# Optimization experiments

Hardware: AMD Instinct MI355X
Metric: run time of the kernel (lower is better)

## Reference

```python
import jax, jax.numpy as jnp
import numpy as np

DIM = 1024
NUM_HEADS = 16
HEAD_DIM = DIM // NUM_HEADS


def setup_inputs() -> dict:
    key = jax.random.key(0)
    k1, k2, k3 = jax.random.split(key, 3)
    x = jax.random.normal(k1, (4, 1024, DIM), dtype=jnp.float32)
    # match nn.Linear init scale roughly: small weights
    Wqkv = jax.random.normal(k2, (3 * DIM, DIM), dtype=jnp.float32) * (1.0 / np.sqrt(DIM))
    Wproj = jax.random.normal(k3, (DIM, DIM), dtype=jnp.float32) * (1.0 / np.sqrt(DIM))
    bproj = jnp.zeros((DIM,), dtype=jnp.float32)
    return {"x": x, "Wqkv": Wqkv, "Wproj": Wproj, "bproj": bproj}


def reference(x, Wqkv, Wproj, bproj):
    bsz, tsz, chans = x.shape
    # fused QKV projection (qkv_bias=False): [B,T,3C]
    qkv = jnp.einsum("btc,oc->bto", x, Wqkv)
    qkv = qkv.reshape(bsz, tsz, 3, NUM_HEADS, HEAD_DIM)
    q = qkv[:, :, 0].transpose(0, 2, 1, 3)  # [B,H,T,D]
    k = qkv[:, :, 1].transpose(0, 2, 1, 3)
    v = qkv[:, :, 2].transpose(0, 2, 1, 3)
    scale = 1.0 / np.sqrt(HEAD_DIM)
    logits = jnp.einsum("bhqd,bhkd->bhqk", q, k) * scale  # [B,H,T,T]
    attn = jax.nn.softmax(logits, axis=-1)
    out = jnp.einsum("bhqk,bhkd->bhqd", attn, v)  # [B,H,T,D]
    out = out.transpose(0, 2, 1, 3).reshape(bsz, tsz, chans)
    return jnp.einsum("btc,oc->bto", out, Wproj) + bproj
```

## Files before the change

### kernel.cpp

```cpp
#include <hip/hip_runtime.h>
#include <hip/hip_bf16.h>

typedef __attribute__((ext_vector_type(8))) short bfrag8;
typedef __attribute__((ext_vector_type(4))) short bfrag4;
typedef __attribute__((ext_vector_type(4))) float floatx4;

typedef unsigned short ushort_t;
typedef unsigned int uint_t;

static __device__ __forceinline__ uint_t pk_bf16(float a, float b) {
    union { __hip_bfloat162 h; uint_t u; } cv;
    cv.h = __float22bfloat162_rn(make_float2(a, b));
    return cv.u;
}

#if __has_builtin(__builtin_amdgcn_mfma_f32_16x16x16_bf16)
static __device__ __forceinline__ floatx4 mfma16(bfrag4 a, bfrag4 b, floatx4 c) {
    return __builtin_amdgcn_mfma_f32_16x16x16_bf16(a, b, c, 0, 0, 0);
}
#elif __has_builtin(__builtin_amdgcn_mfma_f32_16x16x16bf16_1k)
static __device__ __forceinline__ floatx4 mfma16(bfrag4 a, bfrag4 b, floatx4 c) {
    return __builtin_amdgcn_mfma_f32_16x16x16bf16_1k(a, b, c, 0, 0, 0);
}
#else
static __device__ __forceinline__ floatx4 mfma16(bfrag4 a, bfrag4 b, floatx4 c) {
    bfrag8 az = {a[0], 0, a[1], 0, a[2], 0, a[3], 0};
    bfrag8 bz = {b[0], 0, b[1], 0, b[2], 0, b[3], 0};
    return __builtin_amdgcn_mfma_f32_16x16x32_bf16(az, bz, c, 0, 0, 0);
}
#endif

static __device__ __forceinline__ void gl_lds16(const ushort_t* g, ushort_t* l) {
    __builtin_amdgcn_global_load_lds(
        (const __attribute__((address_space(1))) void*)g,
        (__attribute__((address_space(3))) void*)l, 16, 0, 0);
}

__global__ __launch_bounds__(256)
void cvt_all(const float* __restrict__ x, const float* __restrict__ wqkv,
             const float* __restrict__ wproj, ushort_t* __restrict__ xb,
             ushort_t* __restrict__ wqkvb, ushort_t* __restrict__ wprojb) {
    int blk = blockIdx.x;
    const float* src; ushort_t* dst; int base;
    if (blk < 4096)      { src = x;     dst = xb;     base = blk; }
    else if (blk < 7168) { src = wqkv;  dst = wqkvb;  base = blk - 4096; }
    else                 { src = wproj; dst = wprojb; base = blk - 7168; }
    int i = (base * 256 + threadIdx.x) * 4;
    float4 f = *(const float4*)(src + i);
    uint_t lo = pk_bf16(f.x, f.y);
    uint_t hi = pk_bf16(f.z, f.w);
    uint2 u = {lo, hi};
    *(uint2*)(dst + i) = u;
}

__global__ __launch_bounds__(256, 2)
void qkv_gemm(const ushort_t* __restrict__ A, const ushort_t* __restrict__ B,
              ushort_t* __restrict__ qp, ushort_t* __restrict__ kp,
              ushort_t* __restrict__ vp) {
    const int K = 1024;
    __shared__ ushort_t As[128 * 64];
    __shared__ ushort_t Bs[128 * 64];
    int tid = threadIdx.x;
    int wave = __builtin_amdgcn_readfirstlane(tid >> 6);
    int lane = tid & 63;
    int quad = lane >> 4, l16 = lane & 15;
    int wm = (wave >> 1) * 64, wn = (wave & 1) * 64;
    int m0 = blockIdx.y * 128, n0 = blockIdx.x * 128;

    int rl = lane >> 3;
    int gc = (lane & 7) ^ rl;

    floatx4 acc[4][4] = {};

    const ushort_t* Ag = A + (size_t)m0 * K;
    const ushort_t* Bg = B + (size_t)n0 * K;

    for (int k0 = 0; k0 < K; k0 += 64) {
        __syncthreads();
#pragma unroll
        for (int i = 0; i < 4; i++) {
            int row = wave * 32 + i * 8 + rl;
            gl_lds16(Ag + (size_t)row * K + k0 + gc * 8, &As[(wave * 32 + i * 8) * 64]);
            gl_lds16(Bg + (size_t)row * K + k0 + gc * 8, &Bs[(wave * 32 + i * 8) * 64]);
        }
        __syncthreads();
#pragma unroll
        for (int ks = 0; ks < 2; ks++) {
            bfrag8 af[4], bf[4];
#pragma unroll
            for (int mt = 0; mt < 4; mt++) {
                int r = wm + mt * 16 + l16;
                af[mt] = *(const bfrag8*)&As[r * 64 + ((4 * ks + quad) ^ (r & 7)) * 8];
            }
#pragma unroll
            for (int nt = 0; nt < 4; nt++) {
                int r = wn + nt * 16 + l16;
                bf[nt] = *(const bfrag8*)&Bs[r * 64 + ((4 * ks + quad) ^ (r & 7)) * 8];
            }
#pragma unroll
            for (int mt = 0; mt < 4; mt++)
#pragma unroll
                for (int nt = 0; nt < 4; nt++)
                    acc[mt][nt] = __builtin_amdgcn_mfma_f32_16x16x32_bf16(
                        af[mt], bf[nt], acc[mt][nt], 0, 0, 0);
        }
    }

#pragma unroll
    for (int mt = 0; mt < 4; mt++) {
#pragma unroll
        for (int nt = 0; nt < 4; nt++) {
            int o = n0 + wn + nt * 16 + l16;
            int s = o >> 10;
            int rem = o & 1023;
            int h = rem >> 6, d = rem & 63;
            ushort_t* dst = (s == 0) ? qp : (s == 1) ? kp : vp;
            float scl = (s == 0) ? 0.125f : 1.0f;
            uint_t p01 = pk_bf16(acc[mt][nt][0] * scl, acc[mt][nt][1] * scl);
            uint_t p23 = pk_bf16(acc[mt][nt][2] * scl, acc[mt][nt][3] * scl);
            ushort_t pv[4] = {(ushort_t)p01, (ushort_t)(p01 >> 16),
                              (ushort_t)p23, (ushort_t)(p23 >> 16)};
#pragma unroll
            for (int r = 0; r < 4; r++) {
                int t = m0 + wm + mt * 16 + quad * 4 + r;
                int b = t >> 10, tt = t & 1023;
                dst[((size_t)(b * 16 + h) * 1024 + tt) * 64 + d] = pv[r];
            }
        }
    }
}

__global__ __launch_bounds__(256)
void transpose_v(const ushort_t* __restrict__ v, ushort_t* __restrict__ vT) {
    int bh = blockIdx.y;
    int t0 = blockIdx.x * 64;
    __shared__ ushort_t tile[64][72];
    int tid = threadIdx.x;
    int r = tid >> 3;
    int c = (tid & 7) * 8;
#pragma unroll
    for (int i = 0; i < 2; i++) {
        int t = r + i * 32;
        *(uint4*)&tile[t][c] = *(const uint4*)&v[((size_t)bh * 1024 + t0 + t) * 64 + c];
    }
    __syncthreads();
#pragma unroll
    for (int i = 0; i < 2; i++) {
        int d = r + i * 32;
        union { ushort_t u[8]; uint4 v4; } tmp;
#pragma unroll
        for (int j = 0; j < 8; j++) tmp.u[j] = tile[c + j][d];
        *(uint4*)&vT[((size_t)bh * 64 + d) * 1024 + t0 + c] = tmp.v4;
    }
}

__global__ __launch_bounds__(256, 2)
void attn_kernel(const ushort_t* __restrict__ q, const ushort_t* __restrict__ k,
                 const ushort_t* __restrict__ vT, ushort_t* __restrict__ out) {
    int id = blockIdx.x;
    int bh = (id & 7) + ((id >> 6) << 3);
    int qt = (id >> 3) & 7;
    const ushort_t* qb = q + (size_t)bh * 1024 * 64;
    const ushort_t* kb = k + (size_t)bh * 1024 * 64;
    const ushort_t* vtb = vT + (size_t)bh * 64 * 1024;
    int tid = threadIdx.x;
    int wave = __builtin_amdgcn_readfirstlane(tid >> 6);
    int lane = tid & 63;
    int quad = lane >> 4, l16 = lane & 15;
    int q0 = qt * 128 + wave * 32;

    __shared__ ushort_t Ks[128 * 64];
    __shared__ ushort_t VTs[64 * 136];

    int rl = lane >> 3;
    int gc = (lane & 7) ^ rl;

    bfrag8 qf[2][2];
#pragma unroll
    for (int mt = 0; mt < 2; mt++)
#pragma unroll
        for (int ks = 0; ks < 2; ks++)
            qf[mt][ks] = *(const bfrag8*)&qb[(size_t)(q0 + mt * 16 + l16) * 64 + ks * 32 + quad * 8];

    floatx4 oacc[2][4] = {};
    float li[2] = {0.f, 0.f};

    int vd = tid >> 2;
    int vc = tid & 3;

    for (int kt = 0; kt < 8; kt++) {
        uint4 vv[4];
#pragma unroll
        for (int i = 0; i < 4; i++)
            vv[i] = *(const uint4*)&vtb[(size_t)vd * 1024 + kt * 128 + (vc + i * 4) * 8];
        __syncthreads();
#pragma unroll
        for (int i = 0; i < 4; i++) {
            int row = wave * 32 + i * 8 + rl;
            gl_lds16(kb + (size_t)(kt * 128 + row) * 64 + gc * 8, &Ks[(wave * 32 + i * 8) * 64]);
        }
#pragma unroll
        for (int i = 0; i < 4; i++)
            *(uint4*)&VTs[vd * 136 + (vc + i * 4) * 8] = vv[i];
        __syncthreads();

#pragma unroll
        for (int half = 0; half < 2; half++) {
            floatx4 st[2][4] = {};
#pragma unroll
            for (int ks = 0; ks < 2; ks++) {
                bfrag8 kf[4];
#pragma unroll
                for (int tt = 0; tt < 4; tt++) {
                    int r = (half * 4 + tt) * 16 + l16;
                    kf[tt] = *(const bfrag8*)&Ks[r * 64 + ((4 * ks + quad) ^ (r & 7)) * 8];
                }
#pragma unroll
                for (int mt = 0; mt < 2; mt++)
#pragma unroll
                    for (int tt = 0; tt < 4; tt++)
                        st[mt][tt] = __builtin_amdgcn_mfma_f32_16x16x32_bf16(
                            kf[tt], qf[mt][ks], st[mt][tt], 0, 0, 0);
            }

            bfrag4 pf[2][4];
#pragma unroll
            for (int mt = 0; mt < 2; mt++)
#pragma unroll
                for (int tt = 0; tt < 4; tt++) {
                    float p0 = __expf(st[mt][tt][0]);
                    float p1 = __expf(st[mt][tt][1]);
                    float p2 = __expf(st[mt][tt][2]);
                    float p3 = __expf(st[mt][tt][3]);
                    li[mt] += (p0 + p1) + (p2 + p3);
                    union { uint2 u; bfrag4 f; } pk;
                    pk.u.x = pk_bf16(p0, p1);
                    pk.u.y = pk_bf16(p2, p3);
                    pf[mt][tt] = pk.f;
                }

#pragma unroll
            for (int tt = 0; tt < 4; tt++) {
                int keyoff = (half * 4 + tt) * 16;
                bfrag4 vb[4];
#pragma unroll
                for (int nd = 0; nd < 4; nd++)
                    vb[nd] = *(const bfrag4*)&VTs[(nd * 16 + l16) * 136 + keyoff + quad * 4];
#pragma unroll
                for (int mt = 0; mt < 2; mt++)
#pragma unroll
                    for (int nd = 0; nd < 4; nd++)
                        oacc[mt][nd] = mfma16(pf[mt][tt], vb[nd], oacc[mt][nd]);
            }
        }
    }

    float inv[2][4];
#pragma unroll
    for (int mt = 0; mt < 2; mt++) {
        float s0 = li[mt];
        s0 += __shfl_xor(s0, 16);
        s0 += __shfl_xor(s0, 32);
#pragma unroll
        for (int r = 0; r < 4; r++)
            inv[mt][r] = 1.0f / __shfl(s0, quad * 4 + r);
    }

    int b = bh >> 4, h = bh & 15;
#pragma unroll
    for (int mt = 0; mt < 2; mt++)
#pragma unroll
        for (int nd = 0; nd < 4; nd++) {
            uint_t c01 = pk_bf16(oacc[mt][nd][0] * inv[mt][0], oacc[mt][nd][1] * inv[mt][1]);
            uint_t c23 = pk_bf16(oacc[mt][nd][2] * inv[mt][2], oacc[mt][nd][3] * inv[mt][3]);
            ushort_t pv[4] = {(ushort_t)c01, (ushort_t)(c01 >> 16),
                              (ushort_t)c23, (ushort_t)(c23 >> 16)};
#pragma unroll
            for (int r = 0; r < 4; r++) {
                int t = q0 + mt * 16 + quad * 4 + r;
                int c = h * 64 + nd * 16 + l16;
                out[((size_t)(b * 1024 + t)) * 1024 + c] = pv[r];
            }
        }
}

__global__ __launch_bounds__(256, 2)
void proj_gemm(const ushort_t* __restrict__ A, const ushort_t* __restrict__ B,
               const float* __restrict__ bias, float* __restrict__ out) {
    const int K = 1024;
    __shared__ ushort_t As[64 * 64];
    __shared__ ushort_t Bs[128 * 64];
    int tid = threadIdx.x;
    int wave = __builtin_amdgcn_readfirstlane(tid >> 6);
    int lane = tid & 63;
    int quad = lane >> 4, l16 = lane & 15;
    int wm = (wave >> 1) * 32, wn = (wave & 1) * 64;
    int m0 = blockIdx.y * 64, n0 = blockIdx.x * 128;

    int rl = lane >> 3;
    int gc = (lane & 7) ^ rl;

    floatx4 acc[2][4] = {};

    const ushort_t* Ag = A + (size_t)m0 * K;
    const ushort_t* Bg = B + (size_t)n0 * K;

    for (int k0 = 0; k0 < K; k0 += 64) {
        __syncthreads();
#pragma unroll
        for (int i = 0; i < 2; i++) {
            int row = wave * 16 + i * 8 + rl;
            gl_lds16(Ag + (size_t)row * K + k0 + gc * 8, &As[(wave * 16 + i * 8) * 64]);
        }
#pragma unroll
        for (int i = 0; i < 4; i++) {
            int row = wave * 32 + i * 8 + rl;
            gl_lds16(Bg + (size_t)row * K + k0 + gc * 8, &Bs[(wave * 32 + i * 8) * 64]);
        }
        __syncthreads();
#pragma unroll
        for (int ks = 0; ks < 2; ks++) {
            bfrag8 af[2], bf[4];
#pragma unroll
            for (int mt = 0; mt < 2; mt++) {
                int r = wm + mt * 16 + l16;
                af[mt] = *(const bfrag8*)&As[r * 64 + ((4 * ks + quad) ^ (r & 7)) * 8];
            }
#pragma unroll
            for (int nt = 0; nt < 4; nt++) {
                int r = wn + nt * 16 + l16;
                bf[nt] = *(const bfrag8*)&Bs[r * 64 + ((4 * ks + quad) ^ (r & 7)) * 8];
            }
#pragma unroll
            for (int mt = 0; mt < 2; mt++)
#pragma unroll
                for (int nt = 0; nt < 4; nt++)
                    acc[mt][nt] = __builtin_amdgcn_mfma_f32_16x16x32_bf16(
                        af[mt], bf[nt], acc[mt][nt], 0, 0, 0);
        }
    }

#pragma unroll
    for (int mt = 0; mt < 2; mt++) {
#pragma unroll
        for (int nt = 0; nt < 4; nt++) {
            int o = n0 + wn + nt * 16 + l16;
            float bv = bias[o];
#pragma unroll
            for (int r = 0; r < 4; r++) {
                int t = m0 + wm + mt * 16 + quad * 4 + r;
                out[(size_t)t * 1024 + o] = acc[mt][nt][r] + bv;
            }
        }
    }
}

extern "C" void kernel_launch(void* const* d_in, const int* in_sizes, int n_in,
                              void* d_out, int out_size, void* d_ws, size_t ws_size,
                              hipStream_t stream) {
    const float* x     = (const float*)d_in[0];
    const float* Wqkv  = (const float*)d_in[1];
    const float* Wproj = (const float*)d_in[2];
    const float* bproj = (const float*)d_in[3];
    float* out = (float*)d_out;

    char* ws = (char*)d_ws;
    ushort_t* xb     = (ushort_t*)(ws);
    ushort_t* wqkvb  = (ushort_t*)(ws + ((size_t)8 << 20));
    ushort_t* wprojb = (ushort_t*)(ws + ((size_t)14 << 20));
    ushort_t* qp     = (ushort_t*)(ws + ((size_t)16 << 20));
    ushort_t* kp     = (ushort_t*)(ws + ((size_t)24 << 20));
    ushort_t* vp     = (ushort_t*)(ws + ((size_t)32 << 20));
    ushort_t* vTp    = (ushort_t*)(ws + ((size_t)40 << 20));
    ushort_t* attn   = (ushort_t*)(ws + ((size_t)48 << 20));

    cvt_all<<<8192, 256, 0, stream>>>(x, Wqkv, Wproj, xb, wqkvb, wprojb);
    qkv_gemm<<<dim3(24, 32), 256, 0, stream>>>(xb, wqkvb, qp, kp, vp);
    transpose_v<<<dim3(16, 64), 256, 0, stream>>>(vp, vTp);
    attn_kernel<<<512, 256, 0, stream>>>(qp, kp, vTp, attn);
    proj_gemm<<<dim3(8, 64), 256, 0, stream>>>(attn, wprojb, bproj, out);
}
```

Before: 169.1 us.

## Fuse V transpose into QKV GEMM epilogue and drop transpose kernel

The QKV GEMM epilogue now writes V directly in transposed [B,H,D,T] layout with 8-byte packed stores, so the separate transpose_v kernel and its round trip through global memory go away. Q/K blocks take a uniform per-block branch instead of per-element selection. The launch bounds hint rises to 3 blocks per CU, and the VT shared-memory row padding shrinks from 136 to 132. The risks are register spills from the tighter occupancy target and changed LDS bank-conflict behaviour in the attention kernel.

```diff
diff --git a/kernel.cpp b/kernel.cpp
--- a/kernel.cpp
+++ b/kernel.cpp
@@ -7,6 +7,7 @@
 
 typedef unsigned short ushort_t;
 typedef unsigned int uint_t;
+typedef unsigned long long u64_t;
 
 static __device__ __forceinline__ uint_t pk_bf16(float a, float b) {
     union { __hip_bfloat162 h; uint_t u; } cv;
@@ -53,10 +54,10 @@
     *(uint2*)(dst + i) = u;
 }
 
-__global__ __launch_bounds__(256, 2)
+__global__ __launch_bounds__(256, 3)
 void qkv_gemm(const ushort_t* __restrict__ A, const ushort_t* __restrict__ B,
               ushort_t* __restrict__ qp, ushort_t* __restrict__ kp,
-              ushort_t* __restrict__ vp) {
+              ushort_t* __restrict__ vTp) {
     const int K = 1024;
     __shared__ ushort_t As[128 * 64];
     __shared__ ushort_t Bs[128 * 64];
@@ -106,51 +107,43 @@
         }
     }
 
-#pragma unroll
-    for (int mt = 0; mt < 4; mt++) {
-#pragma unroll
-        for (int nt = 0; nt < 4; nt++) {
-            int o = n0 + wn + nt * 16 + l16;
-            int s = o >> 10;
-            int rem = o & 1023;
-            int h = rem >> 6, d = rem & 63;
-            ushort_t* dst = (s == 0) ? qp : (s == 1) ? kp : vp;
-            float scl = (s == 0) ? 0.125f : 1.0f;
-            uint_t p01 = pk_bf16(acc[mt][nt][0] * scl, acc[mt][nt][1] * scl);
-            uint_t p23 = pk_bf16(acc[mt][nt][2] * scl, acc[mt][nt][3] * scl);
-            ushort_t pv[4] = {(ushort_t)p01, (ushort_t)(p01 >> 16),
-                              (ushort_t)p23, (ushort_t)(p23 >> 16)};
-#pragma unroll
-            for (int r = 0; r < 4; r++) {
-                int t = m0 + wm + mt * 16 + quad * 4 + r;
-                int b = t >> 10, tt = t & 1023;
-                dst[((size_t)(b * 16 + h) * 1024 + tt) * 64 + d] = pv[r];
-            }
-        }
-    }
-}
-
-__global__ __launch_bounds__(256)
-void transpose_v(const ushort_t* __restrict__ v, ushort_t* __restrict__ vT) {
-    int bh = blockIdx.y;
-    int t0 = blockIdx.x * 64;
-    __shared__ ushort_t tile[64][72];
-    int tid = threadIdx.x;
-    int r = tid >> 3;
-    int c = (tid & 7) * 8;
-#pragma unroll
-    for (int i = 0; i < 2; i++) {
-        int t = r + i * 32;
-        *(uint4*)&tile[t][c] = *(const uint4*)&v[((size_t)bh * 1024 + t0 + t) * 64 + c];
-    }
-    __syncthreads();
-#pragma unroll
-    for (int i = 0; i < 2; i++) {
-        int d = r + i * 32;
-        union { ushort_t u[8]; uint4 v4; } tmp;
-#pragma unroll
-        for (int j = 0; j < 8; j++) tmp.u[j] = tile[c + j][d];
-        *(uint4*)&vT[((size_t)bh * 64 + d) * 1024 + t0 + c] = tmp.v4;
+    int s = n0 >> 10;
+    if (s < 2) {
+        ushort_t* dst = (s == 0) ? qp : kp;
+        float scl = (s == 0) ? 0.125f : 1.0f;
+#pragma unroll
+        for (int mt = 0; mt < 4; mt++) {
+#pragma unroll
+            for (int nt = 0; nt < 4; nt++) {
+                int o = (n0 & 1023) + wn + nt * 16 + l16;
+                int h = o >> 6, d = o & 63;
+                uint_t p01 = pk_bf16(acc[mt][nt][0] * scl, acc[mt][nt][1] * scl);
+                uint_t p23 = pk_bf16(acc[mt][nt][2] * scl, acc[mt][nt][3] * scl);
+                ushort_t pv[4] = {(ushort_t)p01, (ushort_t)(p01 >> 16),
+                                  (ushort_t)p23, (ushort_t)(p23 >> 16)};
+#pragma unroll
+                for (int r = 0; r < 4; r++) {
+                    int t = m0 + wm + mt * 16 + quad * 4 + r;
+                    int b = t >> 10, tt = t & 1023;
+                    dst[((size_t)(b * 16 + h) * 1024 + tt) * 64 + d] = pv[r];
+                }
+            }
+        }
+    } else {
+#pragma unroll
+        for (int mt = 0; mt < 4; mt++) {
+            int t = m0 + wm + mt * 16 + quad * 4;
+            int b = t >> 10, tt = t & 1023;
+#pragma unroll
+            for (int nt = 0; nt < 4; nt++) {
+                int o = (n0 & 1023) + wn + nt * 16 + l16;
+                int h = o >> 6, d = o & 63;
+                uint_t p01 = pk_bf16(acc[mt][nt][0], acc[mt][nt][1]);
+                uint_t p23 = pk_bf16(acc[mt][nt][2], acc[mt][nt][3]);
+                u64_t pk = ((u64_t)p23 << 32) | p01;
+                *(u64_t*)&vTp[((size_t)(b * 16 + h) * 64 + d) * 1024 + tt] = pk;
+            }
+        }
     }
 }
 
@@ -170,7 +163,7 @@
     int q0 = qt * 128 + wave * 32;
 
     __shared__ ushort_t Ks[128 * 64];
-    __shared__ ushort_t VTs[64 * 136];
+    __shared__ ushort_t VTs[64 * 132];
 
     int rl = lane >> 3;
     int gc = (lane & 7) ^ rl;
@@ -201,7 +194,7 @@
         }
 #pragma unroll
         for (int i = 0; i < 4; i++)
-            *(uint4*)&VTs[vd * 136 + (vc + i * 4) * 8] = vv[i];
+            *(uint4*)&VTs[vd * 132 + (vc + i * 4) * 8] = vv[i];
         __syncthreads();
 
 #pragma unroll
@@ -245,7 +238,7 @@
                 bfrag4 vb[4];
 #pragma unroll
                 for (int nd = 0; nd < 4; nd++)
-                    vb[nd] = *(const bfrag4*)&VTs[(nd * 16 + l16) * 136 + keyoff + quad * 4];
+                    vb[nd] = *(const bfrag4*)&VTs[(nd * 16 + l16) * 132 + keyoff + quad * 4];
 #pragma unroll
                 for (int mt = 0; mt < 2; mt++)
 #pragma unroll
@@ -370,13 +363,11 @@
     ushort_t* wprojb = (ushort_t*)(ws + ((size_t)14 << 20));
     ushort_t* qp     = (ushort_t*)(ws + ((size_t)16 << 20));
     ushort_t* kp     = (ushort_t*)(ws + ((size_t)24 << 20));
-    ushort_t* vp     = (ushort_t*)(ws + ((size_t)32 << 20));
     ushort_t* vTp    = (ushort_t*)(ws + ((size_t)40 << 20));
     ushort_t* attn   = (ushort_t*)(ws + ((size_t)48 << 20));
 
     cvt_all<<<8192, 256, 0, stream>>>(x, Wqkv, Wproj, xb, wqkvb, wprojb);
-    qkv_gemm<<<dim3(24, 32), 256, 0, stream>>>(xb, wqkvb, qp, kp, vp);
-    transpose_v<<<dim3(16, 64), 256, 0, stream>>>(vp, vTp);
+    qkv_gemm<<<dim3(24, 32), 256, 0, stream>>>(xb, wqkvb, qp, kp, vTp);
     attn_kernel<<<512, 256, 0, stream>>>(qp, kp, vTp, attn);
     proj_gemm<<<dim3(8, 64), 256, 0, stream>>>(attn, wprojb, bproj, out);
 }
```

Measured after the change: 157.9 us. 1.07x faster.
